# Kernel tuning notes

Hardware: AMD Instinct MI355X
Metric: run time of the kernel (lower is better)

The kernel has to match this reference:

```python
import jax, jax.numpy as jnp
import numpy as np

N_HEAD = 16
ROPE_THETA = 10000.0


def _rope_cache(T, dim, theta=ROPE_THETA):
    # inv_freq over even indices, as in RotaryEmbedding
    inv_freq = 1.0 / (theta ** (jnp.arange(0, dim, 2, dtype=jnp.float32) / dim))
    freqs = jnp.arange(T, dtype=jnp.float32)[:, None] * inv_freq[None, :]  # [T, dim//2]
    return jnp.cos(freqs), jnp.sin(freqs)


def _apply_rope(x, cos, sin):
    # x: [B, H, T, D]; cos/sin: [T, D//2] broadcast over B,H
    x1 = x[..., ::2]
    x2 = x[..., 1::2]
    # even slots: x1*cos - x2*sin ; odd slots: x2*cos + x1*sin (interleaved rotate-pairs)
    r1 = x1 * cos - x2 * sin
    r2 = x2 * cos + x1 * sin
    return jnp.stack([r1, r2], axis=-1).reshape(x.shape)


def setup_inputs() -> dict:
    key = jax.random.key(0)
    k1, k2, k3 = jax.random.split(key, 3)
    B, T, C = 4, 2048, 1024
    x = jax.random.normal(k1, (B, T, C), dtype=jnp.float32)
    W_qkv = jax.random.normal(k2, (C, 3 * C), dtype=jnp.float32) * (C ** -0.5)
    W_out = jax.random.normal(k3, (C, C), dtype=jnp.float32) * (C ** -0.5)
    return {"x": x, "W_qkv": W_qkv, "W_out": W_out}


def reference(x, W_qkv, W_out):
    B, T, C = x.shape
    H = N_HEAD
    D = C // H
    # fused QKV projection -> [3, B, H, T, D]
    qkv = (x @ W_qkv).reshape(B, T, 3, H, D).transpose(2, 0, 3, 1, 4)
    q, k, v = qkv[0], qkv[1], qkv[2]
    cos, sin = _rope_cache(T, D)
    q = _apply_rope(q, cos, sin)
    k = _apply_rope(k, cos, sin)
    scale = 1.0 / jnp.sqrt(jnp.float32(D))
    scores = jnp.einsum('bhqd,bhkd->bhqk', q, k) * scale  # [B,H,T,T]
    causal_mask = jnp.tril(jnp.ones((T, T), dtype=bool))
    scores = jnp.where(causal_mask, scores, -jnp.inf)
    attn = jax.nn.softmax(scores, axis=-1)
    out = jnp.einsum('bhqk,bhkd->bhqd', attn, v)  # [B,H,T,D]
    out = out.transpose(0, 2, 1, 3).reshape(B, T, C)
    return out @ W_out
```

## Files before the change

kernel.cpp:

```cpp
#include <hip/hip_runtime.h>
#include <hip/hip_bf16.h>
#include <math.h>

#define BATCH 4
#define SEQ   2048
#define CDIM  1024
#define NHEAD 16
#define HDIM  64
#define QKVN  3072
#define QSCALE 0.1803368801111244f

typedef float f32x4 __attribute__((ext_vector_type(4)));
typedef float f32x16 __attribute__((ext_vector_type(16)));
typedef short bf16x8 __attribute__((ext_vector_type(8)));
typedef short bf16x4 __attribute__((ext_vector_type(4)));
typedef int i32x2 __attribute__((ext_vector_type(2)));
typedef int i32x4 __attribute__((ext_vector_type(4)));

static __device__ __forceinline__ unsigned short f2bf(float f) {
    unsigned int u = __float_as_uint(f);
    u += 0x7FFF + ((u >> 16) & 1);
    return (unsigned short)(u >> 16);
}
static __device__ __forceinline__ float bf2f(unsigned short u) {
    return __uint_as_float(((unsigned int)u) << 16);
}
static __device__ __forceinline__ unsigned int pk2bf(float lo, float hi) {
    __hip_bfloat162 h = __float22bfloat162_rn(make_float2(lo, hi));
    return *(unsigned int*)&h;
}
static __device__ __forceinline__ bf16x8 lds_read8(const unsigned short* p) {
    bf16x4 lo = *(const bf16x4*)p;
    bf16x4 hi = *(const bf16x4*)(p + 4);
    return __builtin_shufflevector(lo, hi, 0, 1, 2, 3, 4, 5, 6, 7);
}

static __device__ __forceinline__ void transpose_tile(
    const float* __restrict__ W, unsigned short* __restrict__ Wt,
    int K, int N, int bx, int by, unsigned short (*tile)[65], int tid) {
    const int n0 = bx * 64;
    const int k0 = by * 64;
    const int r = tid >> 4;
    const int c4 = (tid & 15) << 2;
    #pragma unroll
    for (int ii = 0; ii < 4; ii++) {
        int row = r + 16 * ii;
        float4 v = *(const float4*)&W[(size_t)(k0 + row) * N + n0 + c4];
        tile[c4 + 0][row] = f2bf(v.x);
        tile[c4 + 1][row] = f2bf(v.y);
        tile[c4 + 2][row] = f2bf(v.z);
        tile[c4 + 3][row] = f2bf(v.w);
    }
    __syncthreads();
    #pragma unroll
    for (int ii = 0; ii < 4; ii++) {
        int row = r + 16 * ii;
        ushort4 o;
        o.x = tile[row][c4 + 0];
        o.y = tile[row][c4 + 1];
        o.z = tile[row][c4 + 2];
        o.w = tile[row][c4 + 3];
        *(ushort4*)&Wt[(size_t)(n0 + row) * K + k0 + c4] = o;
    }
}

__global__ __launch_bounds__(256) void prep(
    const float* __restrict__ x, const float* __restrict__ W_qkv,
    const float* __restrict__ W_out, float2* __restrict__ ctab,
    unsigned short* __restrict__ xb, unsigned short* __restrict__ wqb,
    unsigned short* __restrict__ wob) {
    __shared__ unsigned short tile[64][65];
    const int blk = blockIdx.x;
    const int tid = threadIdx.x;
    if (blk < 8192) {
        const int i = blk * 256 + tid;
        float4 v = ((const float4*)x)[i];
        ushort4 o;
        o.x = f2bf(v.x); o.y = f2bf(v.y); o.z = f2bf(v.z); o.w = f2bf(v.w);
        ((ushort4*)xb)[i] = o;
    } else if (blk < 8448) {
        const int i = (blk - 8192) * 256 + tid;
        const int dp = i & 31;
        const int t = i >> 5;
        const float invf = powf(10000.0f, -((float)(2 * dp)) / 64.0f);
        float sv, cv;
        __sincosf((float)t * invf, &sv, &cv);
        ctab[i] = make_float2(cv, sv);
    } else if (blk < 9216) {
        const int r = blk - 8448;
        transpose_tile(W_qkv, wqb, CDIM, QKVN, r % 48, r / 48, tile, tid);
    } else {
        const int r = blk - 9216;
        transpose_tile(W_out, wob, CDIM, CDIM, r % 16, r / 16, tile, tid);
    }
}

#define GLDS(gp, lp) __builtin_amdgcn_global_load_lds(                       \
    (const __attribute__((address_space(1))) unsigned int*)(gp),             \
    (__attribute__((address_space(3))) unsigned int*)(lp), 16, 0, 0)

template <typename OUT>
__global__ __launch_bounds__(256) void gemm_bt_bf16(
    const unsigned short* __restrict__ A,
    const unsigned short* __restrict__ Bt,
    OUT* __restrict__ C, int M, int N, int K) {
    __shared__ unsigned short As[128 * 64];
    __shared__ unsigned short Bs[128 * 64];

    const int tid = threadIdx.x;
    const int wave = tid >> 6;
    const int lane = tid & 63;
    const int bm = blockIdx.y * 128;
    const int bn = blockIdx.x * 128;
    const int wm = (wave >> 1) * 64;
    const int wn = (wave & 1) * 64;

    const int sr = tid >> 3;
    const int sc = ((tid & 7) ^ (sr & 7)) << 3;
    const unsigned short* Ag = A + (size_t)(bm + sr) * K + sc;
    const unsigned short* Bg = Bt + (size_t)(bn + sr) * K + sc;
    char* AsW = (char*)As + wave * 1024;
    char* BsW = (char*)Bs + wave * 1024;

    const int fm = lane & 15;
    const int quad = lane >> 4;
    const int sl0 = ((quad ^ (fm & 7)) << 3);
    const int sl1 = (((4 + quad) ^ (fm & 7)) << 3);

    f32x4 acc[4][4];
    #pragma unroll
    for (int i = 0; i < 4; i++)
        #pragma unroll
        for (int j = 0; j < 4; j++)
            acc[i][j] = (f32x4){0.f, 0.f, 0.f, 0.f};

    for (int k0 = 0; k0 < K; k0 += 64) {
        GLDS(Ag + k0, AsW);
        GLDS(Ag + 32 * K + k0, AsW + 4096);
        GLDS(Ag + 64 * K + k0, AsW + 8192);
        GLDS(Ag + 96 * K + k0, AsW + 12288);
        GLDS(Bg + k0, BsW);
        GLDS(Bg + 32 * K + k0, BsW + 4096);
        GLDS(Bg + 64 * K + k0, BsW + 8192);
        GLDS(Bg + 96 * K + k0, BsW + 12288);
        __syncthreads();

        bf16x8 af[4], bfr[4];
        #pragma unroll
        for (int i = 0; i < 4; i++)
            af[i] = *(const bf16x8*)&As[(wm + i * 16 + fm) * 64 + sl0];
        #pragma unroll
        for (int j = 0; j < 4; j++)
            bfr[j] = *(const bf16x8*)&Bs[(wn + j * 16 + fm) * 64 + sl0];
        #pragma unroll
        for (int i = 0; i < 4; i++)
            #pragma unroll
            for (int j = 0; j < 4; j++)
                acc[i][j] = __builtin_amdgcn_mfma_f32_16x16x32_bf16(
                    af[i], bfr[j], acc[i][j], 0, 0, 0);
        #pragma unroll
        for (int i = 0; i < 4; i++)
            af[i] = *(const bf16x8*)&As[(wm + i * 16 + fm) * 64 + sl1];
        #pragma unroll
        for (int j = 0; j < 4; j++)
            bfr[j] = *(const bf16x8*)&Bs[(wn + j * 16 + fm) * 64 + sl1];
        #pragma unroll
        for (int i = 0; i < 4; i++)
            #pragma unroll
            for (int j = 0; j < 4; j++)
                acc[i][j] = __builtin_amdgcn_mfma_f32_16x16x32_bf16(
                    af[i], bfr[j], acc[i][j], 0, 0, 0);
        __syncthreads();
    }

    const int er = quad * 4;
    #pragma unroll
    for (int i = 0; i < 4; i++) {
        #pragma unroll
        for (int j = 0; j < 4; j++) {
            #pragma unroll
            for (int r = 0; r < 4; r++) {
                size_t off = (size_t)(bm + wm + i * 16 + er + r) * N + bn + wn + j * 16 + fm;
                if constexpr (sizeof(OUT) == 2)
                    C[off] = f2bf(acc[i][j][r]);
                else
                    C[off] = acc[i][j][r];
            }
        }
    }
}

__global__ __launch_bounds__(256) void gemm_qkv_fused(
    const unsigned short* __restrict__ A,
    const unsigned short* __restrict__ Bt,
    const float2* __restrict__ ctab,
    unsigned short* __restrict__ Qg,
    unsigned short* __restrict__ Kg,
    unsigned short* __restrict__ Vtg) {
    __shared__ unsigned short SH[16384];
    unsigned short* As = SH;
    unsigned short* Bs = SH + 8192;
    const int K = CDIM;

    const int tid = threadIdx.x;
    const int wave = tid >> 6;
    const int lane = tid & 63;
    const int bm = blockIdx.y * 128;
    const int bn = blockIdx.x * 128;
    const int wm = (wave >> 1) * 64;
    const int wn = (wave & 1) * 64;

    const int sr = tid >> 3;
    const int sc = ((tid & 7) ^ (sr & 7)) << 3;
    const unsigned short* Ag = A + (size_t)(bm + sr) * K + sc;
    const unsigned short* Bg = Bt + (size_t)(bn + sr) * K + sc;
    char* AsW = (char*)SH + wave * 1024;
    char* BsW = (char*)SH + 16384 + wave * 1024;

    const int fm = lane & 15;
    const int quad = lane >> 4;
    const int sl0 = ((quad ^ (fm & 7)) << 3);
    const int sl1 = (((4 + quad) ^ (fm & 7)) << 3);

    f32x4 acc[4][4];
    #pragma unroll
    for (int i = 0; i < 4; i++)
        #pragma unroll
        for (int j = 0; j < 4; j++)
            acc[i][j] = (f32x4){0.f, 0.f, 0.f, 0.f};

    for (int k0 = 0; k0 < K; k0 += 64) {
        GLDS(Ag + k0, AsW);
        GLDS(Ag + 32 * K + k0, AsW + 4096);
        GLDS(Ag + 64 * K + k0, AsW + 8192);
        GLDS(Ag + 96 * K + k0, AsW + 12288);
        GLDS(Bg + k0, BsW);
        GLDS(Bg + 32 * K + k0, BsW + 4096);
        GLDS(Bg + 64 * K + k0, BsW + 8192);
        GLDS(Bg + 96 * K + k0, BsW + 12288);
        __syncthreads();

        bf16x8 af[4], bfr[4];
        #pragma unroll
        for (int i = 0; i < 4; i++)
            af[i] = *(const bf16x8*)&As[(wm + i * 16 + fm) * 64 + sl0];
        #pragma unroll
        for (int j = 0; j < 4; j++)
            bfr[j] = *(const bf16x8*)&Bs[(wn + j * 16 + fm) * 64 + sl0];
        #pragma unroll
        for (int i = 0; i < 4; i++)
            #pragma unroll
            for (int j = 0; j < 4; j++)
                acc[i][j] = __builtin_amdgcn_mfma_f32_16x16x32_bf16(
                    af[i], bfr[j], acc[i][j], 0, 0, 0);
        #pragma unroll
        for (int i = 0; i < 4; i++)
            af[i] = *(const bf16x8*)&As[(wm + i * 16 + fm) * 64 + sl1];
        #pragma unroll
        for (int j = 0; j < 4; j++)
            bfr[j] = *(const bf16x8*)&Bs[(wn + j * 16 + fm) * 64 + sl1];
        #pragma unroll
        for (int i = 0; i < 4; i++)
            #pragma unroll
            for (int j = 0; j < 4; j++)
                acc[i][j] = __builtin_amdgcn_mfma_f32_16x16x32_bf16(
                    af[i], bfr[j], acc[i][j], 0, 0, 0);
        __syncthreads();
    }

    const int s = bn >> 10;
    const int hbase = (bn & 1023) >> 6;
    const int b = bm >> 11;
    const int t0 = bm & 2047;

    #pragma unroll 1
    for (int pass = 0; pass < 2; pass++) {
        if ((wave >> 1) == pass) {
            #pragma unroll
            for (int i = 0; i < 4; i++)
                #pragma unroll
                for (int j = 0; j < 4; j++)
                    #pragma unroll
                    for (int r = 0; r < 4; r++)
                        SH[(i * 16 + quad * 4 + r) * 132 + wn + j * 16 + fm] =
                            f2bf(acc[i][j][r]);
        }
        __syncthreads();

        if (s < 2) {
            unsigned short* dst = (s == 0) ? Qg : Kg;
            const float sc2 = (s == 0) ? QSCALE : 1.0f;
            #pragma unroll
            for (int it = 0; it < 16; it++) {
                const int idx = it * 256 + tid;
                const int row = idx >> 6;
                const int col = (idx & 63) << 1;
                const unsigned int pr = *(const unsigned int*)&SH[row * 132 + col];
                const float x0 = bf2f((unsigned short)pr);
                const float x1 = bf2f((unsigned short)(pr >> 16));
                const int t = t0 + pass * 64 + row;
                const int h = hbase + (col >> 6);
                const int d = col & 63;
                const float2 cs = ctab[t * 32 + (d >> 1)];
                const float r0 = (x0 * cs.x - x1 * cs.y) * sc2;
                const float r1 = (x1 * cs.x + x0 * cs.y) * sc2;
                *(unsigned int*)&dst[((size_t)(b * NHEAD + h) * SEQ + t) * HDIM + d] =
                    pk2bf(r0, r1);
            }
        } else {
            #pragma unroll
            for (int it = 0; it < 8; it++) {
                const int idx = it * 256 + tid;
                const int dcol = idx >> 4;
                const int tq = idx & 15;
                ushort4 o;
                o.x = SH[(tq * 4 + 0) * 132 + dcol];
                o.y = SH[(tq * 4 + 1) * 132 + dcol];
                o.z = SH[(tq * 4 + 2) * 132 + dcol];
                o.w = SH[(tq * 4 + 3) * 132 + dcol];
                const int h = hbase + (dcol >> 6);
                const int dl = dcol & 63;
                const int t = t0 + pass * 64 + tq * 4;
                *(ushort4*)&Vtg[((size_t)(b * NHEAD + h) * HDIM + dl) * SEQ + t] = o;
            }
        }
        __syncthreads();
    }
}

__global__ __launch_bounds__(256, 4) void flash_attn_mfma(
    const unsigned short* __restrict__ Qg,
    const unsigned short* __restrict__ Kg,
    const unsigned short* __restrict__ Vtg,
    unsigned short* __restrict__ att) {
    __shared__ unsigned short Ks[2][64 * 68];
    __shared__ unsigned short Vt[2][64 * 68];

    const int tid = threadIdx.x;
    const int wave = tid >> 6;
    const int lane = tid & 63;
    const int l31 = lane & 31;
    const int hi = lane >> 5;
    const int wq = wave * 32;
    const int bh = blockIdx.x & 63;
    const int qt = 15 - (blockIdx.x >> 6);
    const int b = bh >> 4, h = bh & 15;

    const int r_ld = tid >> 4;
    const int c4 = (tid & 15) << 2;

    const unsigned short* Kbase = Kg + (size_t)bh * SEQ * HDIM;
    const unsigned short* Vbase = Vtg + (size_t)bh * HDIM * SEQ;

    const int qrow = qt * 128 + wq + l31;

    bf16x8 bq[4];
    #pragma unroll
    for (int dc = 0; dc < 4; dc++)
        bq[dc] = *(const bf16x8*)&Qg[((size_t)bh * SEQ + qrow) * HDIM + dc * 16 + hi * 8];

    f32x16 O[2];
    #pragma unroll
    for (int nt = 0; nt < 2; nt++)
        #pragma unroll
        for (int r = 0; r < 16; r++) O[nt][r] = 0.f;
    float lsum = 0.f;

    const int jtop = 2 * qt + 1;

    ushort4 kreg[4], vreg[4];
    #pragma unroll
    for (int ii = 0; ii < 4; ii++) {
        const int row = r_ld + 16 * ii;
        kreg[ii] = *(const ushort4*)&Kbase[(size_t)row * HDIM + c4];
        vreg[ii] = *(const ushort4*)&Vbase[(size_t)row * SEQ + c4];
    }
    #pragma unroll
    for (int ii = 0; ii < 4; ii++) {
        const int row = r_ld + 16 * ii;
        *(ushort4*)&Ks[0][row * 68 + c4] = kreg[ii];
        *(ushort4*)&Vt[0][row * 68 + c4] = vreg[ii];
    }
    __syncthreads();

    int cur = 0;
    #pragma unroll 1
    for (int j = 0; j <= jtop; j++) {
        if (j < jtop) {
            #pragma unroll
            for (int ii = 0; ii < 4; ii++) {
                const int row = r_ld + 16 * ii;
                kreg[ii] = *(const ushort4*)&Kbase[(size_t)((j + 1) * 64 + row) * HDIM + c4];
                vreg[ii] = *(const ushort4*)&Vbase[(size_t)row * SEQ + (j + 1) * 64 + c4];
            }
        }

        const bool active = (j * 64) <= (qt * 128 + wq + 31);
        if (active) {
            const unsigned short* Kc = Ks[cur];
            const unsigned short* Vc = Vt[cur];
            const bool diag = (j * 64 + 63) > (qt * 128 + wq);

            #pragma unroll
            for (int kt = 0; kt < 2; kt++) {
                f32x16 sa;
                #pragma unroll
                for (int r = 0; r < 16; r++) sa[r] = 0.f;
                __builtin_amdgcn_s_setprio(1);
                #pragma unroll
                for (int dc = 0; dc < 4; dc++) {
                    bf16x8 ak = lds_read8(&Kc[(kt * 32 + l31) * 68 + dc * 16 + hi * 8]);
                    sa = __builtin_amdgcn_mfma_f32_32x32x16_bf16(ak, bq[dc], sa, 0, 0, 0);
                }
                __builtin_amdgcn_s_setprio(0);

                if (diag) {
                    const int kb = j * 64 + kt * 32 + 4 * hi;
                    #pragma unroll
                    for (int r = 0; r < 16; r++) {
                        const int kg = kb + (r & 3) + 8 * (r >> 2);
                        if (kg > qrow) sa[r] = -INFINITY;
                    }
                }

                float e[16];
                #pragma unroll
                for (int r = 0; r < 16; r++) {
                    e[r] = exp2f(sa[r]);
                    lsum += e[r];
                }
                unsigned int p32[8];
                #pragma unroll
                for (int v = 0; v < 8; v++)
                    p32[v] = pk2bf(e[2 * v], e[2 * v + 1]);

                #pragma unroll
                for (int c = 0; c < 2; c++) {
                    i32x2 s0 = __builtin_amdgcn_permlane32_swap(
                        (int)p32[4 * c + 0], (int)p32[4 * c + 2], false, false);
                    i32x2 s1 = __builtin_amdgcn_permlane32_swap(
                        (int)p32[4 * c + 1], (int)p32[4 * c + 3], false, false);
                    i32x4 pw = (i32x4){s0[0], s1[0], s0[1], s1[1]};
                    bf16x8 pa = *(bf16x8*)&pw;
                    __builtin_amdgcn_s_setprio(1);
                    #pragma unroll
                    for (int nt = 0; nt < 2; nt++) {
                        bf16x8 bv = lds_read8(&Vc[(nt * 32 + l31) * 68 + kt * 32 + c * 16 + hi * 8]);
                        O[nt] = __builtin_amdgcn_mfma_f32_32x32x16_bf16(pa, bv, O[nt], 0, 0, 0);
                    }
                    __builtin_amdgcn_s_setprio(0);
                }
            }
        }

        if (j < jtop) {
            const int nb = cur ^ 1;
            #pragma unroll
            for (int ii = 0; ii < 4; ii++) {
                const int row = r_ld + 16 * ii;
                *(ushort4*)&Ks[nb][row * 68 + c4] = kreg[ii];
                *(ushort4*)&Vt[nb][row * 68 + c4] = vreg[ii];
            }
        }

        __syncthreads();
        cur ^= 1;
    }

    const float lfull = lsum + __shfl_xor(lsum, 32);
    const float inv = 1.0f / lfull;
    #pragma unroll
    for (int r = 0; r < 16; r++) {
        const int qloc = (r & 3) + 8 * (r >> 2) + 4 * hi;
        const float invr = __uint_as_float((unsigned int)__builtin_amdgcn_ds_bpermute(
            qloc * 4, (int)__float_as_uint(inv)));
        const int row = qt * 128 + wq + qloc;
        #pragma unroll
        for (int nt = 0; nt < 2; nt++)
            att[(size_t)(b * SEQ + row) * CDIM + h * HDIM + nt * 32 + l31] =
                f2bf(O[nt][r] * invr);
    }
}

extern "C" void kernel_launch(void* const* d_in, const int* in_sizes, int n_in,
                              void* d_out, int out_size, void* d_ws, size_t ws_size,
                              hipStream_t stream) {
    const float* x     = (const float*)d_in[0];
    const float* W_qkv = (const float*)d_in[1];
    const float* W_out = (const float*)d_in[2];
    float* out = (float*)d_out;

    const int M = BATCH * SEQ;

    float2* ctab = (float2*)d_ws;
    unsigned short* xb   = (unsigned short*)(ctab + SEQ * 32);
    unsigned short* wqb  = xb + (size_t)M * CDIM;
    unsigned short* wob  = wqb + (size_t)CDIM * QKVN;
    unsigned short* attb = wob + (size_t)CDIM * CDIM;
    unsigned short* Qg   = attb + (size_t)M * CDIM;
    unsigned short* Kg   = Qg + (size_t)M * CDIM;
    unsigned short* Vtg  = Kg + (size_t)M * CDIM;

    prep<<<9472, 256, 0, stream>>>(x, W_qkv, W_out, ctab, xb, wqb, wob);

    gemm_qkv_fused<<<dim3(QKVN / 128, M / 128), 256, 0, stream>>>(
        xb, wqb, ctab, Qg, Kg, Vtg);

    flash_attn_mfma<<<BATCH * NHEAD * (SEQ / 128), 256, 0, stream>>>(Qg, Kg, Vtg, attb);

    gemm_bt_bf16<float><<<dim3(CDIM / 128, M / 128), 256, 0, stream>>>(
        attb, wob, out, M, CDIM, CDIM);
}
```

Baseline: 297.8 us.

## Halve GEMM K-tile to 32 and raise occupancy hint for fused QKV GEMM

The generic bf16 GEMM now stages 32-wide K slices instead of 64, with a matching XOR swizzle for the smaller LDS rows. This halves shared memory per block, which can allow more resident blocks. The cost is twice as many barriers and loop iterations per K. The fused QKV GEMM also gets a launch_bounds minimum of 4 blocks per CU, which may force register spilling.

```diff
diff --git a/kernel.cpp b/kernel.cpp
--- a/kernel.cpp
+++ b/kernel.cpp
@@ -104,8 +104,8 @@
     const unsigned short* __restrict__ A,
     const unsigned short* __restrict__ Bt,
     OUT* __restrict__ C, int M, int N, int K) {
-    __shared__ unsigned short As[128 * 64];
-    __shared__ unsigned short Bs[128 * 64];
+    __shared__ unsigned short As[128 * 32];
+    __shared__ unsigned short Bs[128 * 32];
 
     const int tid = threadIdx.x;
     const int wave = tid >> 6;
@@ -115,17 +115,18 @@
     const int wm = (wave >> 1) * 64;
     const int wn = (wave & 1) * 64;
 
-    const int sr = tid >> 3;
-    const int sc = ((tid & 7) ^ (sr & 7)) << 3;
-    const unsigned short* Ag = A + (size_t)(bm + sr) * K + sc;
-    const unsigned short* Bg = Bt + (size_t)(bn + sr) * K + sc;
+    const int srow = tid >> 2;
+    const int scol = (((tid & 3) ^ ((tid >> 3) & 3)) << 3);
+    const unsigned short* Ag0 = A + (size_t)(bm + srow) * K + scol;
+    const unsigned short* Ag1 = A + (size_t)(bm + 64 + srow) * K + scol;
+    const unsigned short* Bg0 = Bt + (size_t)(bn + srow) * K + scol;
+    const unsigned short* Bg1 = Bt + (size_t)(bn + 64 + srow) * K + scol;
     char* AsW = (char*)As + wave * 1024;
     char* BsW = (char*)Bs + wave * 1024;
 
     const int fm = lane & 15;
     const int quad = lane >> 4;
-    const int sl0 = ((quad ^ (fm & 7)) << 3);
-    const int sl1 = (((4 + quad) ^ (fm & 7)) << 3);
+    const int ck = (quad ^ ((fm >> 1) & 3)) << 3;
 
     f32x4 acc[4][4];
     #pragma unroll
@@ -134,36 +135,20 @@
         for (int j = 0; j < 4; j++)
             acc[i][j] = (f32x4){0.f, 0.f, 0.f, 0.f};
 
-    for (int k0 = 0; k0 < K; k0 += 64) {
-        GLDS(Ag + k0, AsW);
-        GLDS(Ag + 32 * K + k0, AsW + 4096);
-        GLDS(Ag + 64 * K + k0, AsW + 8192);
-        GLDS(Ag + 96 * K + k0, AsW + 12288);
-        GLDS(Bg + k0, BsW);
-        GLDS(Bg + 32 * K + k0, BsW + 4096);
-        GLDS(Bg + 64 * K + k0, BsW + 8192);
-        GLDS(Bg + 96 * K + k0, BsW + 12288);
+    for (int k0 = 0; k0 < K; k0 += 32) {
+        GLDS(Ag0 + k0, AsW);
+        GLDS(Ag1 + k0, AsW + 4096);
+        GLDS(Bg0 + k0, BsW);
+        GLDS(Bg1 + k0, BsW + 4096);
         __syncthreads();
 
         bf16x8 af[4], bfr[4];
         #pragma unroll
         for (int i = 0; i < 4; i++)
-            af[i] = *(const bf16x8*)&As[(wm + i * 16 + fm) * 64 + sl0];
+            af[i] = *(const bf16x8*)&As[(wm + i * 16 + fm) * 32 + ck];
         #pragma unroll
         for (int j = 0; j < 4; j++)
-            bfr[j] = *(const bf16x8*)&Bs[(wn + j * 16 + fm) * 64 + sl0];
-        #pragma unroll
-        for (int i = 0; i < 4; i++)
-            #pragma unroll
-            for (int j = 0; j < 4; j++)
-                acc[i][j] = __builtin_amdgcn_mfma_f32_16x16x32_bf16(
-                    af[i], bfr[j], acc[i][j], 0, 0, 0);
-        #pragma unroll
-        for (int i = 0; i < 4; i++)
-            af[i] = *(const bf16x8*)&As[(wm + i * 16 + fm) * 64 + sl1];
-        #pragma unroll
-        for (int j = 0; j < 4; j++)
-            bfr[j] = *(const bf16x8*)&Bs[(wn + j * 16 + fm) * 64 + sl1];
+            bfr[j] = *(const bf16x8*)&Bs[(wn + j * 16 + fm) * 32 + ck];
         #pragma unroll
         for (int i = 0; i < 4; i++)
             #pragma unroll
@@ -190,7 +175,7 @@
     }
 }
 
-__global__ __launch_bounds__(256) void gemm_qkv_fused(
+__global__ __launch_bounds__(256, 4) void gemm_qkv_fused(
     const unsigned short* __restrict__ A,
     const unsigned short* __restrict__ Bt,
     const float2* __restrict__ ctab,
```

Measured after the change: 270.4 us. 9.2% less time.
